# Optimization experiments

Hardware: AMD Instinct MI355X
Metric: run time of the kernel (lower is better)

## Reference

```python
import jax, jax.numpy as jnp
import numpy as np

B, T, DE, DR, H = 8192, 8, 512, 1024, 1024


def setup_inputs() -> dict:
    key = jax.random.key(0)
    ks = jax.random.split(key, 8)
    std = 1.0 / np.sqrt(H)
    u = lambda k, shape: jax.random.uniform(k, shape, jnp.float32, -std, std)
    return {
        "entity": jax.random.normal(ks[0], (B, T, DE), jnp.float32),
        "relation": jax.random.normal(ks[1], (B, T, DR), jnp.float32),
        "We": u(ks[2], (H, DE)),
        "be": u(ks[3], (H,)),
        "Wr": u(ks[4], (H, DR)),
        "br": u(ks[5], (H,)),
        "Wh": u(ks[6], (H, H)),
        "bh": u(ks[7], (H,)),
    }


def reference(entity, relation, We, be, Wr, br, Wh, bh):
    # entity: [B, T, DE], relation: [B, T, DR]
    # Precompute time-parallel input projections (linear, math-equivalent to per-step).
    g = (jnp.einsum("btd,hd->bth", entity, We) + be
         + jnp.einsum("btd,hd->bth", relation, Wr) + br)  # [B, T, H]

    def step(h, gt):
        h = jax.nn.relu(gt + h @ Wh.T + bh)  # RNNCell_rel: relu(e2h(e)+r2h(r)+h2h(h))
        return h, h

    h0 = jnp.zeros((entity.shape[0], Wh.shape[0]), entity.dtype)
    hn, outs = jax.lax.scan(step, h0, jnp.transpose(g, (1, 0, 2)))  # outs: [T, B, H]
    output = jnp.transpose(outs, (1, 0, 2))  # [B, T, H] (batch-first)
    need = hn.T  # faithful to hidden[0].transpose(0,1): [H, B]
    return output, need
```

## Files before the change

kernel.cpp:

```cpp
#include <hip/hip_runtime.h>
#include <hip/hip_bf16.h>

#define BB 8192
#define TT 8
#define DEe 512
#define DRr 1024
#define HH 1024
#define KTOT 2560

typedef __attribute__((ext_vector_type(8))) __bf16 bf16x8;
typedef __attribute__((ext_vector_type(4))) __bf16 bf16x4;
typedef __attribute__((ext_vector_type(4))) float f32x4;

__device__ __forceinline__ void gld_lds16(const __bf16* g, __bf16* l) {
    __builtin_amdgcn_global_load_lds(
        (const __attribute__((address_space(1))) void*)g,
        (__attribute__((address_space(3))) void*)l, 16, 0, 0);
}

__global__ void pack_a(const float* __restrict__ ent, const float* __restrict__ rel,
                       __bf16* __restrict__ buf, int t) {
    const int b = blockIdx.y;
    const int sec = blockIdx.x;
    const int i = threadIdx.x;
    float4 v; size_t dst;
    if (sec == 0) {
        v = *(const float4*)(ent + ((size_t)b * TT + t) * DEe + i * 4);
        dst = (size_t)b * KTOT + i * 4;
    } else {
        int d = (sec - 1) * 512 + i * 4;
        v = *(const float4*)(rel + ((size_t)b * TT + t) * DRr + d);
        dst = (size_t)b * KTOT + DEe + d;
    }
    bf16x4 o = {(__bf16)v.x, (__bf16)v.y, (__bf16)v.z, (__bf16)v.w};
    *(bf16x4*)(buf + dst) = o;
}

__global__ void pack_b(const float* __restrict__ We, const float* __restrict__ Wr,
                       const float* __restrict__ Wh, __bf16* __restrict__ Bw) {
    const int n = blockIdx.y;
    const int sec = blockIdx.x;
    const int i = threadIdx.x;
    float4 v; size_t dst;
    if (sec == 0) {
        v = *(const float4*)(We + (size_t)n * DEe + i * 4);
        dst = (size_t)n * KTOT + i * 4;
    } else if (sec <= 2) {
        int d = (sec - 1) * 512 + i * 4;
        v = *(const float4*)(Wr + (size_t)n * DRr + d);
        dst = (size_t)n * KTOT + DEe + d;
    } else {
        int d = (sec - 3) * 512 + i * 4;
        v = *(const float4*)(Wh + (size_t)n * HH + d);
        dst = (size_t)n * KTOT + 1536 + d;
    }
    bf16x4 o = {(__bf16)v.x, (__bf16)v.y, (__bf16)v.z, (__bf16)v.w};
    *(bf16x4*)(Bw + dst) = o;
}

__global__ __launch_bounds__(256) void gemm_step(
    const __bf16* __restrict__ A, const __bf16* __restrict__ Bw,
    const float* __restrict__ be, const float* __restrict__ br,
    const float* __restrict__ bh,
    float* __restrict__ out, __bf16* __restrict__ Anext,
    float* __restrict__ need, int K, int t) {
    __shared__ __bf16 sA[128 * 32];
    __shared__ __bf16 sB[128 * 32];
    __shared__ float sBias[128];

    const int tid  = threadIdx.x;
    const int lane = tid & 63;
    const int w    = tid >> 6;
    const int tileM = blockIdx.y * 128;
    const int tileN = blockIdx.x * 128;

    if (tid < 128) {
        int n = tileN + tid;
        sBias[tid] = be[n] + br[n] + bh[n];
    }

    const int r0 = (w * 2 + 0) * 16 + (lane >> 2);
    const int r1 = (w * 2 + 1) * 16 + (lane >> 2);
    const int cc = (lane & 3) * 8;
    const __bf16* gA0 = A + (size_t)(tileM + r0) * KTOT + cc;
    const __bf16* gA1 = A + (size_t)(tileM + r1) * KTOT + cc;
    const __bf16* gB0 = Bw + (size_t)(tileN + r0) * KTOT + cc;
    const __bf16* gB1 = Bw + (size_t)(tileN + r1) * KTOT + cc;
    __bf16* lA0 = sA + (w * 2 + 0) * 512;
    __bf16* lA1 = sA + (w * 2 + 1) * 512;
    __bf16* lB0 = sB + (w * 2 + 0) * 512;
    __bf16* lB1 = sB + (w * 2 + 1) * 512;

    const int wm = (w >> 1) * 64, wn = (w & 1) * 64;
    const int fm = lane & 15, fq = lane >> 4;

    f32x4 acc[4][4];
#pragma unroll
    for (int i = 0; i < 4; i++)
#pragma unroll
        for (int j = 0; j < 4; j++) acc[i][j] = {0.f, 0.f, 0.f, 0.f};

    for (int k0 = 0; k0 < K; k0 += 32) {
        gld_lds16(gA0 + k0, lA0);
        gld_lds16(gA1 + k0, lA1);
        gld_lds16(gB0 + k0, lB0);
        gld_lds16(gB1 + k0, lB1);
        __syncthreads();
        bf16x8 af[4], bf[4];
#pragma unroll
        for (int mf = 0; mf < 4; mf++)
            af[mf] = *(const bf16x8*)&sA[(wm + mf * 16 + fm) * 32 + fq * 8];
#pragma unroll
        for (int nf = 0; nf < 4; nf++)
            bf[nf] = *(const bf16x8*)&sB[(wn + nf * 16 + fm) * 32 + fq * 8];
#pragma unroll
        for (int mf = 0; mf < 4; mf++)
#pragma unroll
            for (int nf = 0; nf < 4; nf++)
                acc[mf][nf] = __builtin_amdgcn_mfma_f32_16x16x32_bf16(
                    af[mf], bf[nf], acc[mf][nf], 0, 0, 0);
        __syncthreads();
    }

#pragma unroll
    for (int mf = 0; mf < 4; mf++) {
#pragma unroll
        for (int nf = 0; nf < 4; nf++) {
            f32x4 v = acc[mf][nf];
            const int nl = wn + nf * 16 + fm;
            const int n  = tileN + nl;
            const int m0 = tileM + wm + mf * 16 + fq * 4;
            const float bias = sBias[nl];
            float hv[4];
#pragma unroll
            for (int r = 0; r < 4; r++) {
                float x = v[r] + bias;
                hv[r] = x > 0.f ? x : 0.f;
                out[(size_t)(m0 + r) * (TT * HH) + (size_t)t * HH + n] = hv[r];
                if (Anext)
                    Anext[(size_t)(m0 + r) * KTOT + 1536 + n] = (__bf16)hv[r];
            }
            if (need) {
                f32x4 nv = {hv[0], hv[1], hv[2], hv[3]};
                *(f32x4*)&need[(size_t)n * BB + m0] = nv;
            }
        }
    }
}

extern "C" void kernel_launch(void* const* d_in, const int* in_sizes, int n_in,
                              void* d_out, int out_size, void* d_ws, size_t ws_size,
                              hipStream_t stream) {
    const float* ent = (const float*)d_in[0];
    const float* rel = (const float*)d_in[1];
    const float* We  = (const float*)d_in[2];
    const float* be  = (const float*)d_in[3];
    const float* Wr  = (const float*)d_in[4];
    const float* br  = (const float*)d_in[5];
    const float* Wh  = (const float*)d_in[6];
    const float* bh  = (const float*)d_in[7];

    float* out  = (float*)d_out;
    float* need = out + (size_t)BB * TT * HH;

    char* ws = (char*)d_ws;
    __bf16* buf0 = (__bf16*)ws;
    __bf16* buf1 = (__bf16*)(ws + (size_t)BB * KTOT * 2);
    __bf16* Bw   = (__bf16*)(ws + (size_t)2 * BB * KTOT * 2);
    __bf16* bufs[2] = {buf0, buf1};

    pack_b<<<dim3(5, 1024), 128, 0, stream>>>(We, Wr, Wh, Bw);
    for (int t = 0; t < TT; t++) {
        pack_a<<<dim3(3, BB), 128, 0, stream>>>(ent, rel, bufs[t & 1], t);
        gemm_step<<<dim3(8, 64), 256, 0, stream>>>(
            bufs[t & 1], Bw, be, br, bh, out,
            (t < 7) ? bufs[(t + 1) & 1] : nullptr,
            (t == 7) ? need : nullptr,
            (t == 0) ? 1536 : KTOT, t);
    }
}
```

Measured before the change: 1.144 ms.

## Hoist input projections into one time-batched GEMM, then run recurrent-only steps

Converts all entity/relation inputs to bf16 once and computes the input projection for all time steps in a single large GEMM, storing pre-activations in the output buffer. Each recurrent step then does only the h@Wh GEMM with K=1024, reading the precomputed projection, adding bias and applying relu in the epilogue. Bias summation moves to a tiny precompute kernel. This cuts redundant K work and per-step pack launches, at the cost of an extra fp32 read-modify-write of the output per step.

```diff
diff --git a/kernel.cpp b/kernel.cpp
--- a/kernel.cpp
+++ b/kernel.cpp
@@ -6,7 +6,8 @@
 #define DEe 512
 #define DRr 1024
 #define HH 1024
-#define KTOT 2560
+#define KP 1536
+#define MP 65536
 
 typedef __attribute__((ext_vector_type(8))) __bf16 bf16x8;
 typedef __attribute__((ext_vector_type(4))) __bf16 bf16x4;
@@ -18,52 +19,60 @@
         (__attribute__((address_space(3))) void*)l, 16, 0, 0);
 }
 
-__global__ void pack_a(const float* __restrict__ ent, const float* __restrict__ rel,
-                       __bf16* __restrict__ buf, int t) {
-    const int b = blockIdx.y;
-    const int sec = blockIdx.x;
-    const int i = threadIdx.x;
+__global__ __launch_bounds__(256) void conv_a(const float* __restrict__ ent,
+                                              const float* __restrict__ rel,
+                                              __bf16* __restrict__ Ap) {
+    const size_t NE4 = (size_t)BB * TT * DEe / 4;
+    size_t i = (size_t)blockIdx.x * 256 + threadIdx.x;
     float4 v; size_t dst;
-    if (sec == 0) {
-        v = *(const float4*)(ent + ((size_t)b * TT + t) * DEe + i * 4);
-        dst = (size_t)b * KTOT + i * 4;
+    if (i < NE4) {
+        size_t e = i << 2;
+        v = *(const float4*)(ent + e);
+        dst = (e >> 9) * KP + (e & 511);
     } else {
-        int d = (sec - 1) * 512 + i * 4;
-        v = *(const float4*)(rel + ((size_t)b * TT + t) * DRr + d);
-        dst = (size_t)b * KTOT + DEe + d;
+        size_t e = (i - NE4) << 2;
+        v = *(const float4*)(rel + e);
+        dst = (e >> 10) * KP + 512 + (e & 1023);
     }
     bf16x4 o = {(__bf16)v.x, (__bf16)v.y, (__bf16)v.z, (__bf16)v.w};
-    *(bf16x4*)(buf + dst) = o;
+    *(bf16x4*)(Ap + dst) = o;
 }
 
 __global__ void pack_b(const float* __restrict__ We, const float* __restrict__ Wr,
-                       const float* __restrict__ Wh, __bf16* __restrict__ Bw) {
+                       const float* __restrict__ Wh, __bf16* __restrict__ Bp,
+                       __bf16* __restrict__ Bh) {
     const int n = blockIdx.y;
     const int sec = blockIdx.x;
     const int i = threadIdx.x;
-    float4 v; size_t dst;
+    float4 v; __bf16* dst;
     if (sec == 0) {
         v = *(const float4*)(We + (size_t)n * DEe + i * 4);
-        dst = (size_t)n * KTOT + i * 4;
+        dst = Bp + (size_t)n * KP + i * 4;
     } else if (sec <= 2) {
         int d = (sec - 1) * 512 + i * 4;
         v = *(const float4*)(Wr + (size_t)n * DRr + d);
-        dst = (size_t)n * KTOT + DEe + d;
+        dst = Bp + (size_t)n * KP + 512 + d;
     } else {
         int d = (sec - 3) * 512 + i * 4;
         v = *(const float4*)(Wh + (size_t)n * HH + d);
-        dst = (size_t)n * KTOT + 1536 + d;
+        dst = Bh + (size_t)n * HH + d;
     }
     bf16x4 o = {(__bf16)v.x, (__bf16)v.y, (__bf16)v.z, (__bf16)v.w};
-    *(bf16x4*)(Bw + dst) = o;
-}
-
-__global__ __launch_bounds__(256) void gemm_step(
+    *(bf16x4*)dst = o;
+}
+
+__global__ void bias_k(const float* __restrict__ be, const float* __restrict__ br,
+                       const float* __restrict__ bh, float* __restrict__ bias) {
+    int i = blockIdx.x * 256 + threadIdx.x;
+    if (i < HH) bias[i] = be[i] + br[i] + bh[i];
+}
+
+template <int MODE>
+__global__ __launch_bounds__(256) void gemm(
     const __bf16* __restrict__ A, const __bf16* __restrict__ Bw,
-    const float* __restrict__ be, const float* __restrict__ br,
-    const float* __restrict__ bh,
-    float* __restrict__ out, __bf16* __restrict__ Anext,
-    float* __restrict__ need, int K, int t) {
+    const float* __restrict__ bias, float* __restrict__ out,
+    __bf16* __restrict__ hn, float* __restrict__ need, int t) {
+    constexpr int K = (MODE == 0) ? KP : HH;
     __shared__ __bf16 sA[128 * 32];
     __shared__ __bf16 sB[128 * 32];
     __shared__ float sBias[128];
@@ -74,18 +83,15 @@
     const int tileM = blockIdx.y * 128;
     const int tileN = blockIdx.x * 128;
 
-    if (tid < 128) {
-        int n = tileN + tid;
-        sBias[tid] = be[n] + br[n] + bh[n];
-    }
+    if (tid < 128) sBias[tid] = bias[tileN + tid];
 
     const int r0 = (w * 2 + 0) * 16 + (lane >> 2);
     const int r1 = (w * 2 + 1) * 16 + (lane >> 2);
     const int cc = (lane & 3) * 8;
-    const __bf16* gA0 = A + (size_t)(tileM + r0) * KTOT + cc;
-    const __bf16* gA1 = A + (size_t)(tileM + r1) * KTOT + cc;
-    const __bf16* gB0 = Bw + (size_t)(tileN + r0) * KTOT + cc;
-    const __bf16* gB1 = Bw + (size_t)(tileN + r1) * KTOT + cc;
+    const __bf16* gA0 = A + (size_t)(tileM + r0) * K + cc;
+    const __bf16* gA1 = A + (size_t)(tileM + r1) * K + cc;
+    const __bf16* gB0 = Bw + (size_t)(tileN + r0) * K + cc;
+    const __bf16* gB1 = Bw + (size_t)(tileN + r1) * K + cc;
     __bf16* lA0 = sA + (w * 2 + 0) * 512;
     __bf16* lA1 = sA + (w * 2 + 1) * 512;
     __bf16* lB0 = sB + (w * 2 + 0) * 512;
@@ -130,19 +136,34 @@
             const int nl = wn + nf * 16 + fm;
             const int n  = tileN + nl;
             const int m0 = tileM + wm + mf * 16 + fq * 4;
-            const float bias = sBias[nl];
-            float hv[4];
-#pragma unroll
-            for (int r = 0; r < 4; r++) {
-                float x = v[r] + bias;
-                hv[r] = x > 0.f ? x : 0.f;
-                out[(size_t)(m0 + r) * (TT * HH) + (size_t)t * HH + n] = hv[r];
-                if (Anext)
-                    Anext[(size_t)(m0 + r) * KTOT + 1536 + n] = (__bf16)hv[r];
-            }
-            if (need) {
-                f32x4 nv = {hv[0], hv[1], hv[2], hv[3]};
-                *(f32x4*)&need[(size_t)n * BB + m0] = nv;
+            if (MODE == 0) {
+#pragma unroll
+                for (int r = 0; r < 4; r++) {
+                    int row = m0 + r;
+                    float x = v[r];
+                    if ((row & 7) == 0) {
+                        x += sBias[nl];
+                        x = x > 0.f ? x : 0.f;
+                        hn[(size_t)(row >> 3) * HH + n] = (__bf16)x;
+                    }
+                    out[(size_t)row * HH + n] = x;
+                }
+            } else {
+                float hv[4];
+#pragma unroll
+                for (int r = 0; r < 4; r++) {
+                    int m = m0 + r;
+                    size_t gidx = ((size_t)m * TT + t) * HH + n;
+                    float x = out[gidx] + v[r] + sBias[nl];
+                    x = x > 0.f ? x : 0.f;
+                    hv[r] = x;
+                    out[gidx] = x;
+                    hn[(size_t)m * HH + n] = (__bf16)x;
+                }
+                if (need) {
+                    f32x4 nv = {hv[0], hv[1], hv[2], hv[3]};
+                    *(f32x4*)&need[(size_t)n * BB + m0] = nv;
+                }
             }
         }
     }
@@ -164,18 +185,24 @@
     float* need = out + (size_t)BB * TT * HH;
 
     char* ws = (char*)d_ws;
-    __bf16* buf0 = (__bf16*)ws;
-    __bf16* buf1 = (__bf16*)(ws + (size_t)BB * KTOT * 2);
-    __bf16* Bw   = (__bf16*)(ws + (size_t)2 * BB * KTOT * 2);
-    __bf16* bufs[2] = {buf0, buf1};
-
-    pack_b<<<dim3(5, 1024), 128, 0, stream>>>(We, Wr, Wh, Bw);
-    for (int t = 0; t < TT; t++) {
-        pack_a<<<dim3(3, BB), 128, 0, stream>>>(ent, rel, bufs[t & 1], t);
-        gemm_step<<<dim3(8, 64), 256, 0, stream>>>(
-            bufs[t & 1], Bw, be, br, bh, out,
-            (t < 7) ? bufs[(t + 1) & 1] : nullptr,
-            (t == 7) ? need : nullptr,
-            (t == 0) ? 1536 : KTOT, t);
-    }
-}
+    size_t off = 0;
+    __bf16* Ap = (__bf16*)(ws + off); off += (size_t)MP * KP * 2;
+    __bf16* Bp = (__bf16*)(ws + off); off += (size_t)HH * KP * 2;
+    __bf16* Bh = (__bf16*)(ws + off); off += (size_t)HH * HH * 2;
+    float*  bias = (float*)(ws + off); off += HH * 4;
+    __bf16* hb0 = (__bf16*)(ws + off); off += (size_t)BB * HH * 2;
+    __bf16* hb1 = (__bf16*)(ws + off);
+    __bf16* hb[2] = {hb0, hb1};
+
+    conv_a<<<98304, 256, 0, stream>>>(ent, rel, Ap);
+    pack_b<<<dim3(5, 1024), 128, 0, stream>>>(We, Wr, Wh, Bp, Bh);
+    bias_k<<<4, 256, 0, stream>>>(be, br, bh, bias);
+
+    gemm<0><<<dim3(8, 512), 256, 0, stream>>>(Ap, Bp, bias, out, hb0, nullptr, 0);
+
+    for (int t = 1; t < TT; t++) {
+        gemm<1><<<dim3(8, 64), 256, 0, stream>>>(
+            hb[(t - 1) & 1], Bh, bias, out, hb[t & 1],
+            (t == 7) ? need : nullptr, t);
+    }
+}
```

Result: slower. 1.285 ms (+12.3%).
